# Optimization experiments

Measured on AMD Instinct MI355X. Metric: run time of the kernel, lower is better.

Reference implementation:

```python
import jax, jax.numpy as jnp
import numpy as np

# Graph block sizes (outermost -> innermost), fixed fanout neighbor sampling
N0, N1, N2, N3 = 256000, 25600, 2560, 512
D_IN, D_H, D_OUT = 1024, 256, 19
FANOUTS = (10, 10, 5)


def _lin(key, d_in, d_out):
    return jax.random.normal(key, (d_in, d_out), jnp.float32) / np.sqrt(d_in)


def setup_inputs() -> dict:
    key = jax.random.key(0)
    ks = jax.random.split(key, 13)
    x = jax.random.normal(ks[0], (N0, D_IN), jnp.float32)
    # DGL block convention: dst nodes are the first n_dst src nodes, so
    # h_dst = h[:n_dst]. Neighbor tables index into the src node set.
    nbr0 = jax.random.randint(ks[1], (N1, FANOUTS[0]), 0, N0)
    nbr1 = jax.random.randint(ks[2], (N2, FANOUTS[1]), 0, N1)
    nbr2 = jax.random.randint(ks[3], (N3, FANOUTS[2]), 0, N2)
    return {
        "x": x, "nbr0": nbr0, "nbr1": nbr1, "nbr2": nbr2,
        "Wself0": _lin(ks[4], D_IN, D_H), "Wneigh0": _lin(ks[5], D_IN, D_H),
        "b0": jnp.zeros((D_H,), jnp.float32),
        "Wself1": _lin(ks[6], D_H, D_H), "Wneigh1": _lin(ks[7], D_H, D_H),
        "b1": jnp.zeros((D_H,), jnp.float32),
        "Wself2": _lin(ks[8], D_H, D_OUT), "Wneigh2": _lin(ks[9], D_H, D_OUT),
        "b2": jnp.zeros((D_OUT,), jnp.float32),
    }


def sage_layer(h, nbr, Wself, Wneigh, b):
    # SAGEConv('mean'): fc_self(h_dst) + fc_neigh(mean over sampled neighbors)
    n_dst = nbr.shape[0]
    h_neigh = jnp.mean(h[nbr], axis=1)  # [n_dst, fanout, d] -> [n_dst, d]
    return h[:n_dst] @ Wself + h_neigh @ Wneigh + b


def reference(x, nbr0, nbr1, nbr2,
              Wself0, Wneigh0, b0,
              Wself1, Wneigh1, b1,
              Wself2, Wneigh2, b2):
    # Dropout is identity in eval mode; activation = relu.
    h = jax.nn.relu(sage_layer(x, nbr0, Wself0, Wneigh0, b0))
    h = jax.nn.relu(sage_layer(h, nbr1, Wself1, Wneigh1, b1))
    return sage_layer(h, nbr2, Wself2, Wneigh2, b2)  # [N3, n_classes]
```

## Files before the change

kernel.cpp:

```cpp
#include <hip/hip_runtime.h>
#include <hip/hip_bf16.h>


typedef __attribute__((ext_vector_type(4))) float f32x4;
typedef __attribute__((ext_vector_type(8))) short s16x8;

__device__ __forceinline__ unsigned short f2bf_u16(float f) {
  unsigned int u = __float_as_uint(f);
  u += 0x7fffu + ((u >> 16) & 1u);
  return (unsigned short)(u >> 16);
}

__device__ __forceinline__ float bf2f(unsigned short u) {
  return __uint_as_float(((unsigned int)u) << 16);
}

__global__ void prep_wcat(const float* __restrict__ Wself,
                          const float* __restrict__ Wneigh,
                          unsigned short* __restrict__ Wt, int Khalf, int N) {
  int idx = blockIdx.x * 256 + threadIdx.x;
  int Kc = 2 * Khalf;
  if (idx >= N * Kc) return;
  int n = idx / Kc, k = idx - n * Kc;
  float v = (k < Khalf) ? Wself[(size_t)k * N + n] : Wneigh[(size_t)(k - Khalf) * N + n];
  Wt[idx] = f2bf_u16(v);
}

template <int D, int F>
__global__ void gather_cat(const float* __restrict__ h,
                           const int* __restrict__ nbr,
                           unsigned short* __restrict__ out) {
  const int i = blockIdx.x;
  const int c = threadIdx.x;
  int idx[F];
#pragma unroll
  for (int f = 0; f < F; ++f) idx[f] = nbr[(size_t)i * F + f];
  constexpr float inv = 1.0f / (float)F;

  float4 s = reinterpret_cast<const float4*>(h + (size_t)i * D)[c];
  ushort4 us = {f2bf_u16(s.x), f2bf_u16(s.y), f2bf_u16(s.z), f2bf_u16(s.w)};
  reinterpret_cast<ushort4*>(out + (size_t)i * 2 * D)[c] = us;

  float ax = 0.f, ay = 0.f, az = 0.f, aw = 0.f;
#pragma unroll
  for (int f = 0; f < F; ++f) {
    float4 v = reinterpret_cast<const float4*>(h + (size_t)idx[f] * D)[c];
    ax += v.x; ay += v.y; az += v.z; aw += v.w;
  }
  ushort4 un = {f2bf_u16(ax * inv), f2bf_u16(ay * inv), f2bf_u16(az * inv), f2bf_u16(aw * inv)};
  reinterpret_cast<ushort4*>(out + (size_t)i * 2 * D + D)[c] = un;
}

template <int BM, int BN, int WM, int WN, bool RELU>
__global__ void gemm_bf16(const unsigned short* __restrict__ A,
                          const unsigned short* __restrict__ Bt,
                          const float* __restrict__ bias,
                          float* __restrict__ C,
                          int M, int N, int Kc) {
  constexpr int BK = 32;
  constexpr int LDK = BK + 8;
  constexpr int THREADS = WM * WN * 64;
  constexpr int MF = BM / (WM * 16);
  constexpr int NF = BN / (WN * 16);
  __shared__ __align__(16) unsigned short As[BM][LDK];
  __shared__ __align__(16) unsigned short Bs[BN][LDK];

  const int tid = threadIdx.x;
  const int wid = tid >> 6, lane = tid & 63;
  const int wm = wid / WN, wn = wid % WN;
  const size_t bm = (size_t)blockIdx.x * BM;
  const size_t bn = (size_t)blockIdx.y * BN;

  f32x4 acc[MF][NF];
#pragma unroll
  for (int mi = 0; mi < MF; ++mi)
#pragma unroll
    for (int ni = 0; ni < NF; ++ni)
      acc[mi][ni] = (f32x4){0.f, 0.f, 0.f, 0.f};

  const int arow = tid >> 2;
  const int apart = (tid & 3) * 8;
  const int klo = (lane >> 4) * 8;
  const int l15 = lane & 15;

  for (int kt = 0; kt < Kc; kt += BK) {
#pragma unroll
    for (int r = 0; r < BM; r += THREADS / 4) {
      s16x8 v = *reinterpret_cast<const s16x8*>(A + (bm + r + arow) * (size_t)Kc + kt + apart);
      *reinterpret_cast<s16x8*>(&As[r + arow][apart]) = v;
    }
#pragma unroll
    for (int r = 0; r < BN; r += THREADS / 4) {
      s16x8 v = *reinterpret_cast<const s16x8*>(Bt + (bn + r + arow) * (size_t)Kc + kt + apart);
      *reinterpret_cast<s16x8*>(&Bs[r + arow][apart]) = v;
    }
    __syncthreads();

    s16x8 af[MF], bfr[NF];
#pragma unroll
    for (int mi = 0; mi < MF; ++mi)
      af[mi] = *reinterpret_cast<const s16x8*>(&As[wm * MF * 16 + mi * 16 + l15][klo]);
#pragma unroll
    for (int ni = 0; ni < NF; ++ni)
      bfr[ni] = *reinterpret_cast<const s16x8*>(&Bs[wn * NF * 16 + ni * 16 + l15][klo]);
#pragma unroll
    for (int mi = 0; mi < MF; ++mi)
#pragma unroll
      for (int ni = 0; ni < NF; ++ni)
        acc[mi][ni] = __builtin_amdgcn_mfma_f32_16x16x32_bf16(af[mi], bfr[ni], acc[mi][ni], 0, 0, 0);
    __syncthreads();
  }

  const int rif = (lane >> 4) * 4;
#pragma unroll
  for (int mi = 0; mi < MF; ++mi) {
    size_t r0 = bm + wm * MF * 16 + mi * 16 + rif;
#pragma unroll
    for (int ni = 0; ni < NF; ++ni) {
      int c = (int)bn + wn * NF * 16 + ni * 16 + l15;
      float bv = bias[c];
#pragma unroll
      for (int r = 0; r < 4; ++r) {
        float v = acc[mi][ni][r] + bv;
        if (RELU) v = fmaxf(v, 0.f);
        C[(r0 + r) * (size_t)N + c] = v;
      }
    }
  }
}

__global__ void out_layer(const unsigned short* __restrict__ cat,
                          const float* __restrict__ Ws, const float* __restrict__ Wn,
                          const float* __restrict__ b, float* __restrict__ out) {
  const int i = blockIdx.x, t = threadIdx.x;
  __shared__ float row[512];
  __shared__ float part[8][32];
  row[t]       = bf2f(cat[(size_t)i * 512 + t]);
  row[t + 256] = bf2f(cat[(size_t)i * 512 + t + 256]);
  __syncthreads();
  const int n = t & 31, seg = t >> 5;
  float p = 0.f;
  if (n < 19) {
#pragma unroll
    for (int e = 0; e < 64; ++e) {
      int k = seg * 64 + e;
      float w = (k < 256) ? Ws[k * 19 + n] : Wn[(k - 256) * 19 + n];
      p += row[k] * w;
    }
  }
  part[seg][n] = p;
  __syncthreads();
  if (t < 19) {
    float s = b[t];
#pragma unroll
    for (int g = 0; g < 8; ++g) s += part[g][t];
    out[(size_t)i * 19 + t] = s;
  }
}

extern "C" void kernel_launch(void* const* d_in, const int* in_sizes, int n_in,
                              void* d_out, int out_size, void* d_ws, size_t ws_size,
                              hipStream_t stream) {
  const float* x   = (const float*)d_in[0];
  const int*   nbr0 = (const int*)d_in[1];
  const int*   nbr1 = (const int*)d_in[2];
  const int*   nbr2 = (const int*)d_in[3];
  const float* Ws0 = (const float*)d_in[4];
  const float* Wn0 = (const float*)d_in[5];
  const float* b0  = (const float*)d_in[6];
  const float* Ws1 = (const float*)d_in[7];
  const float* Wn1 = (const float*)d_in[8];
  const float* b1  = (const float*)d_in[9];
  const float* Ws2 = (const float*)d_in[10];
  const float* Wn2 = (const float*)d_in[11];
  const float* b2  = (const float*)d_in[12];
  float* out = (float*)d_out;

  char* ws = (char*)d_ws;
  unsigned short* A0   = (unsigned short*)(ws);
  unsigned short* Wt0  = (unsigned short*)(ws + 104857600);
  float*          h0   = (float*)(ws + 105906176);
  unsigned short* cat1 = (unsigned short*)(ws + 132120576);
  unsigned short* Wt1  = (unsigned short*)(ws + 134742016);
  float*          h1   = (float*)(ws + 135004160);
  unsigned short* cat2 = (unsigned short*)(ws + 137625600);

  prep_wcat<<<(256 * 2048 + 255) / 256, 256, 0, stream>>>(Ws0, Wn0, Wt0, 1024, 256);
  prep_wcat<<<(256 * 512 + 255) / 256, 256, 0, stream>>>(Ws1, Wn1, Wt1, 256, 256);

  gather_cat<1024, 10><<<25600, 256, 0, stream>>>(x, nbr0, A0);
  gemm_bf16<128, 256, 2, 4, true>
      <<<dim3(200, 1), 512, 0, stream>>>(A0, Wt0, b0, h0, 25600, 256, 2048);

  gather_cat<256, 10><<<2560, 64, 0, stream>>>(h0, nbr1, cat1);
  gemm_bf16<64, 128, 2, 2, true>
      <<<dim3(40, 2), 256, 0, stream>>>(cat1, Wt1, b1, h1, 2560, 256, 512);

  gather_cat<256, 5><<<512, 64, 0, stream>>>(h1, nbr2, cat2);
  out_layer<<<512, 256, 0, stream>>>(cat2, Ws2, Wn2, b2, out);
}
```

Measured before the change: 321.8 us.

## Fuse neighbor gather-mean into GEMM A-tile loads and drop concat buffers

The separate gather_cat kernels, which wrote a bf16 concatenated [self|mean-neighbor] matrix to global memory, are replaced by a sage_gemm kernel. It builds each A tile directly from fp32 features, loading the self rows or averaging the neighbor rows on the fly, and converts to bf16 in shared memory. The tile shape becomes BM=64, BN=256, BK=64 with 4 waves, and the last layer gathers from h1 inside out_fused. This removes the round-trip of the large intermediate A matrix and several kernel launches. In exchange, the irregular gather latency now sits inside the GEMM main loop without prefetching, and layer 0 runs only 400 blocks.

New measurement: 577.1 us. 79.3% more time.

```diff
diff --git a/kernel.cpp b/kernel.cpp
--- a/kernel.cpp
+++ b/kernel.cpp
@@ -11,8 +11,13 @@
   return (unsigned short)(u >> 16);
 }
 
-__device__ __forceinline__ float bf2f(unsigned short u) {
-  return __uint_as_float(((unsigned int)u) << 16);
+__device__ __forceinline__ s16x8 pack_bf16x8(const float4& a, const float4& b) {
+  s16x8 w;
+  w[0] = (short)f2bf_u16(a.x); w[1] = (short)f2bf_u16(a.y);
+  w[2] = (short)f2bf_u16(a.z); w[3] = (short)f2bf_u16(a.w);
+  w[4] = (short)f2bf_u16(b.x); w[5] = (short)f2bf_u16(b.y);
+  w[6] = (short)f2bf_u16(b.z); w[7] = (short)f2bf_u16(b.w);
+  return w;
 }
 
 __global__ void prep_wcat(const float* __restrict__ Wself,
@@ -26,176 +31,171 @@
   Wt[idx] = f2bf_u16(v);
 }
 
-template <int D, int F>
-__global__ void gather_cat(const float* __restrict__ h,
-                           const int* __restrict__ nbr,
-                           unsigned short* __restrict__ out) {
-  const int i = blockIdx.x;
-  const int c = threadIdx.x;
-  int idx[F];
-#pragma unroll
-  for (int f = 0; f < F; ++f) idx[f] = nbr[(size_t)i * F + f];
-  constexpr float inv = 1.0f / (float)F;
-
-  float4 s = reinterpret_cast<const float4*>(h + (size_t)i * D)[c];
-  ushort4 us = {f2bf_u16(s.x), f2bf_u16(s.y), f2bf_u16(s.z), f2bf_u16(s.w)};
-  reinterpret_cast<ushort4*>(out + (size_t)i * 2 * D)[c] = us;
-
-  float ax = 0.f, ay = 0.f, az = 0.f, aw = 0.f;
-#pragma unroll
-  for (int f = 0; f < F; ++f) {
-    float4 v = reinterpret_cast<const float4*>(h + (size_t)idx[f] * D)[c];
-    ax += v.x; ay += v.y; az += v.z; aw += v.w;
-  }
-  ushort4 un = {f2bf_u16(ax * inv), f2bf_u16(ay * inv), f2bf_u16(az * inv), f2bf_u16(aw * inv)};
-  reinterpret_cast<ushort4*>(out + (size_t)i * 2 * D + D)[c] = un;
-}
-
-template <int BM, int BN, int WM, int WN, bool RELU>
-__global__ void gemm_bf16(const unsigned short* __restrict__ A,
+template <int D, int F, bool RELU>
+__global__ void sage_gemm(const float* __restrict__ X,
+                          const int* __restrict__ nbr,
                           const unsigned short* __restrict__ Bt,
                           const float* __restrict__ bias,
-                          float* __restrict__ C,
-                          int M, int N, int Kc) {
-  constexpr int BK = 32;
+                          float* __restrict__ C) {
+  constexpr int BM = 64, BN = 256, BK = 64;
   constexpr int LDK = BK + 8;
-  constexpr int THREADS = WM * WN * 64;
-  constexpr int MF = BM / (WM * 16);
-  constexpr int NF = BN / (WN * 16);
+  constexpr int Kc = 2 * D;
   __shared__ __align__(16) unsigned short As[BM][LDK];
   __shared__ __align__(16) unsigned short Bs[BN][LDK];
 
   const int tid = threadIdx.x;
   const int wid = tid >> 6, lane = tid & 63;
-  const int wm = wid / WN, wn = wid % WN;
   const size_t bm = (size_t)blockIdx.x * BM;
-  const size_t bn = (size_t)blockIdx.y * BN;
-
-  f32x4 acc[MF][NF];
-#pragma unroll
-  for (int mi = 0; mi < MF; ++mi)
-#pragma unroll
-    for (int ni = 0; ni < NF; ++ni)
+
+  const int r = tid >> 2;
+  const int coff = (tid & 3) * 16;
+
+  int idx[F];
+#pragma unroll
+  for (int f = 0; f < F; ++f) idx[f] = nbr[(bm + r) * F + f];
+
+  f32x4 acc[4][4];
+#pragma unroll
+  for (int mi = 0; mi < 4; ++mi)
+#pragma unroll
+    for (int ni = 0; ni < 4; ++ni)
       acc[mi][ni] = (f32x4){0.f, 0.f, 0.f, 0.f};
 
-  const int arow = tid >> 2;
-  const int apart = (tid & 3) * 8;
   const int klo = (lane >> 4) * 8;
   const int l15 = lane & 15;
 
   for (int kt = 0; kt < Kc; kt += BK) {
-#pragma unroll
-    for (int r = 0; r < BM; r += THREADS / 4) {
-      s16x8 v = *reinterpret_cast<const s16x8*>(A + (bm + r + arow) * (size_t)Kc + kt + apart);
-      *reinterpret_cast<s16x8*>(&As[r + arow][apart]) = v;
-    }
-#pragma unroll
-    for (int r = 0; r < BN; r += THREADS / 4) {
-      s16x8 v = *reinterpret_cast<const s16x8*>(Bt + (bn + r + arow) * (size_t)Kc + kt + apart);
-      *reinterpret_cast<s16x8*>(&Bs[r + arow][apart]) = v;
+    float4 v0, v1, v2, v3;
+    if (kt < D) {
+      const float4* p = reinterpret_cast<const float4*>(X + (bm + r) * (size_t)D + kt + coff);
+      v0 = p[0]; v1 = p[1]; v2 = p[2]; v3 = p[3];
+    } else {
+      v0 = v1 = v2 = v3 = make_float4(0.f, 0.f, 0.f, 0.f);
+      const int kk = kt - D + coff;
+#pragma unroll
+      for (int f = 0; f < F; ++f) {
+        const float4* p = reinterpret_cast<const float4*>(X + (size_t)idx[f] * D + kk);
+        float4 u0 = p[0], u1 = p[1], u2 = p[2], u3 = p[3];
+        v0.x += u0.x; v0.y += u0.y; v0.z += u0.z; v0.w += u0.w;
+        v1.x += u1.x; v1.y += u1.y; v1.z += u1.z; v1.w += u1.w;
+        v2.x += u2.x; v2.y += u2.y; v2.z += u2.z; v2.w += u2.w;
+        v3.x += u3.x; v3.y += u3.y; v3.z += u3.z; v3.w += u3.w;
+      }
+      constexpr float inv = 1.0f / (float)F;
+      v0.x *= inv; v0.y *= inv; v0.z *= inv; v0.w *= inv;
+      v1.x *= inv; v1.y *= inv; v1.z *= inv; v1.w *= inv;
+      v2.x *= inv; v2.y *= inv; v2.z *= inv; v2.w *= inv;
+      v3.x *= inv; v3.y *= inv; v3.z *= inv; v3.w *= inv;
+    }
+    *reinterpret_cast<s16x8*>(&As[r][coff]) = pack_bf16x8(v0, v1);
+    *reinterpret_cast<s16x8*>(&As[r][coff + 8]) = pack_bf16x8(v2, v3);
+
+#pragma unroll
+    for (int pz = 0; pz < 4; ++pz) {
+      const int row = pz * 64 + r;
+      const s16x8* pb = reinterpret_cast<const s16x8*>(Bt + (size_t)row * Kc + kt + coff);
+      s16x8 b0 = pb[0], b1 = pb[1];
+      *reinterpret_cast<s16x8*>(&Bs[row][coff]) = b0;
+      *reinterpret_cast<s16x8*>(&Bs[row][coff + 8]) = b1;
     }
     __syncthreads();
 
-    s16x8 af[MF], bfr[NF];
-#pragma unroll
-    for (int mi = 0; mi < MF; ++mi)
-      af[mi] = *reinterpret_cast<const s16x8*>(&As[wm * MF * 16 + mi * 16 + l15][klo]);
-#pragma unroll
-    for (int ni = 0; ni < NF; ++ni)
-      bfr[ni] = *reinterpret_cast<const s16x8*>(&Bs[wn * NF * 16 + ni * 16 + l15][klo]);
-#pragma unroll
-    for (int mi = 0; mi < MF; ++mi)
-#pragma unroll
-      for (int ni = 0; ni < NF; ++ni)
-        acc[mi][ni] = __builtin_amdgcn_mfma_f32_16x16x32_bf16(af[mi], bfr[ni], acc[mi][ni], 0, 0, 0);
+#pragma unroll
+    for (int ks = 0; ks < 2; ++ks) {
+      s16x8 af[4], bfr[4];
+#pragma unroll
+      for (int mi = 0; mi < 4; ++mi)
+        af[mi] = *reinterpret_cast<const s16x8*>(&As[mi * 16 + l15][ks * 32 + klo]);
+#pragma unroll
+      for (int ni = 0; ni < 4; ++ni)
+        bfr[ni] = *reinterpret_cast<const s16x8*>(&Bs[wid * 64 + ni * 16 + l15][ks * 32 + klo]);
+#pragma unroll
+      for (int mi = 0; mi < 4; ++mi)
+#pragma unroll
+        for (int ni = 0; ni < 4; ++ni)
+          acc[mi][ni] = __builtin_amdgcn_mfma_f32_16x16x32_bf16(af[mi], bfr[ni], acc[mi][ni], 0, 0, 0);
+    }
     __syncthreads();
   }
 
   const int rif = (lane >> 4) * 4;
 #pragma unroll
-  for (int mi = 0; mi < MF; ++mi) {
-    size_t r0 = bm + wm * MF * 16 + mi * 16 + rif;
-#pragma unroll
-    for (int ni = 0; ni < NF; ++ni) {
-      int c = (int)bn + wn * NF * 16 + ni * 16 + l15;
-      float bv = bias[c];
-#pragma unroll
-      for (int r = 0; r < 4; ++r) {
-        float v = acc[mi][ni][r] + bv;
+  for (int mi = 0; mi < 4; ++mi) {
+    const size_t r0 = bm + mi * 16 + rif;
+#pragma unroll
+    for (int ni = 0; ni < 4; ++ni) {
+      const int c = wid * 64 + ni * 16 + l15;
+      const float bv = bias[c];
+#pragma unroll
+      for (int rr = 0; rr < 4; ++rr) {
+        float v = acc[mi][ni][rr] + bv;
         if (RELU) v = fmaxf(v, 0.f);
-        C[(r0 + r) * (size_t)N + c] = v;
+        C[(r0 + rr) * (size_t)BN + c] = v;
       }
     }
   }
 }
 
-__global__ void out_layer(const unsigned short* __restrict__ cat,
+__global__ void out_fused(const float* __restrict__ h1, const int* __restrict__ nbr,
                           const float* __restrict__ Ws, const float* __restrict__ Wn,
                           const float* __restrict__ b, float* __restrict__ out) {
   const int i = blockIdx.x, t = threadIdx.x;
   __shared__ float row[512];
   __shared__ float part[8][32];
-  row[t]       = bf2f(cat[(size_t)i * 512 + t]);
-  row[t + 256] = bf2f(cat[(size_t)i * 512 + t + 256]);
+  row[t] = h1[(size_t)i * 256 + t];
+  float s = 0.f;
+#pragma unroll
+  for (int f = 0; f < 5; ++f) s += h1[(size_t)nbr[i * 5 + f] * 256 + t];
+  row[256 + t] = s * 0.2f;
   __syncthreads();
   const int n = t & 31, seg = t >> 5;
   float p = 0.f;
   if (n < 19) {
 #pragma unroll
     for (int e = 0; e < 64; ++e) {
-      int k = seg * 64 + e;
-      float w = (k < 256) ? Ws[k * 19 + n] : Wn[(k - 256) * 19 + n];
+      const int k = seg * 64 + e;
+      const float w = (k < 256) ? Ws[k * 19 + n] : Wn[(k - 256) * 19 + n];
       p += row[k] * w;
     }
   }
   part[seg][n] = p;
   __syncthreads();
   if (t < 19) {
-    float s = b[t];
-#pragma unroll
-    for (int g = 0; g < 8; ++g) s += part[g][t];
-    out[(size_t)i * 19 + t] = s;
+    float sm = b[t];
+#pragma unroll
+    for (int g = 0; g < 8; ++g) sm += part[g][t];
+    out[(size_t)i * 19 + t] = sm;
   }
 }
 
 extern "C" void kernel_launch(void* const* d_in, const int* in_sizes, int n_in,
                               void* d_out, int out_size, void* d_ws, size_t ws_size,
                               hipStream_t stream) {
-  const float* x   = (const float*)d_in[0];
+  const float* x    = (const float*)d_in[0];
   const int*   nbr0 = (const int*)d_in[1];
   const int*   nbr1 = (const int*)d_in[2];
   const int*   nbr2 = (const int*)d_in[3];
-  const float* Ws0 = (const float*)d_in[4];
-  const float* Wn0 = (const float*)d_in[5];
-  const float* b0  = (const float*)d_in[6];
-  const float* Ws1 = (const float*)d_in[7];
-  const float* Wn1 = (const float*)d_in[8];
-  const float* b1  = (const float*)d_in[9];
-  const float* Ws2 = (const float*)d_in[10];
-  const float* Wn2 = (const float*)d_in[11];
-  const float* b2  = (const float*)d_in[12];
+  const float* Ws0  = (const float*)d_in[4];
+  const float* Wn0  = (const float*)d_in[5];
+  const float* b0   = (const float*)d_in[6];
+  const float* Ws1  = (const float*)d_in[7];
+  const float* Wn1  = (const float*)d_in[8];
+  const float* b1   = (const float*)d_in[9];
+  const float* Ws2  = (const float*)d_in[10];
+  const float* Wn2  = (const float*)d_in[11];
+  const float* b2   = (const float*)d_in[12];
   float* out = (float*)d_out;
 
   char* ws = (char*)d_ws;
-  unsigned short* A0   = (unsigned short*)(ws);
-  unsigned short* Wt0  = (unsigned short*)(ws + 104857600);
-  float*          h0   = (float*)(ws + 105906176);
-  unsigned short* cat1 = (unsigned short*)(ws + 132120576);
-  unsigned short* Wt1  = (unsigned short*)(ws + 134742016);
-  float*          h1   = (float*)(ws + 135004160);
-  unsigned short* cat2 = (unsigned short*)(ws + 137625600);
+  unsigned short* Wt0 = (unsigned short*)(ws);
+  unsigned short* Wt1 = (unsigned short*)(ws + 1048576);
+  float*          h0  = (float*)(ws + 1310720);
+  float*          h1  = (float*)(ws + 27525120);
 
   prep_wcat<<<(256 * 2048 + 255) / 256, 256, 0, stream>>>(Ws0, Wn0, Wt0, 1024, 256);
   prep_wcat<<<(256 * 512 + 255) / 256, 256, 0, stream>>>(Ws1, Wn1, Wt1, 256, 256);
 
-  gather_cat<1024, 10><<<25600, 256, 0, stream>>>(x, nbr0, A0);
-  gemm_bf16<128, 256, 2, 4, true>
-      <<<dim3(200, 1), 512, 0, stream>>>(A0, Wt0, b0, h0, 25600, 256, 2048);
-
-  gather_cat<256, 10><<<2560, 64, 0, stream>>>(h0, nbr1, cat1);
-  gemm_bf16<64, 128, 2, 2, true>
-      <<<dim3(40, 2), 256, 0, stream>>>(cat1, Wt1, b1, h1, 2560, 256, 512);
-
-  gather_cat<256, 5><<<512, 64, 0, stream>>>(h1, nbr2, cat2);
-  out_layer<<<512, 256, 0, stream>>>(cat2, Ws2, Wn2, b2, out);
-}
+  sage_gemm<1024, 10, true><<<25600 / 64, 256, 0, stream>>>(x, nbr0, Wt0, b0, h0);
+  sage_gemm<256, 10, true><<<2560 / 64, 256, 0, stream>>>(h0, nbr1, Wt1, b1, h1);
+  out_fused<<<512, 256, 0, stream>>>(h1, nbr2, Ws2, Wn2, b2, out);
+}
```
